# Optimization experiments

Measured on AMD Instinct MI355X. Metric: run time of the kernel, lower is better.

## Reference

```python
import jax, jax.numpy as jnp
import numpy as np

L_LAYERS, D, H, FF_MUL = 4, 512, 8, 4
VOCAB, SEQ, MEM, CMEM, RATIO = 32000, 1024, 1024, 256, 4
DH = D // H


def _ln(x, g, b):
    mu = jnp.mean(x, -1, keepdims=True)
    var = jnp.mean((x - mu) ** 2, -1, keepdims=True)
    return (x - mu) / jnp.sqrt(var + 1e-5) * g + b


def _heads(x):
    b, n, _ = x.shape
    return x.reshape(b, n, H, -1).transpose(0, 2, 1, 3)  # [b,h,n,dh]


def _shift(x):
    # relative-position shift trick, x: [b,h,i,j] -> [b,h,i,j]
    b, h, i, j = x.shape
    x = jnp.concatenate([x, jnp.zeros((b, h, i, i), x.dtype)], -1)
    l = i + j - 1
    x = x.reshape(b, h, i * (i + j))
    pad = (-x.shape[-1]) % l
    x = jnp.pad(x, ((0, 0), (0, 0), (0, pad))).reshape(b, h, -1, l)
    return x[:, :, :i, i - 1:]


def _conv(x, w, b):
    # x: [B,L,D], w: [D_out, D_in, RATIO] (OIH), stride=RATIO
    y = jax.lax.conv_general_dilated(x.transpose(0, 2, 1), w, (RATIO,), 'VALID',
                                     dimension_numbers=('NCH', 'OIH', 'NCH'))
    return y.transpose(0, 2, 1) + b


def _full_attn(q, k, v):
    dots = jnp.einsum('bhid,bhjd->bhij', q, k) * (q.shape[-1] ** -0.5)
    return jnp.einsum('bhij,bhjd->bhid', jax.nn.softmax(dots, -1), v)


def setup_inputs() -> dict:
    key = jax.random.key(0)
    ks = jax.random.split(key, 24)
    s = 0.02
    return {
        'seq': jax.random.randint(ks[0], (4, SEQ), 0, VOCAB),
        'mask': jnp.ones((4, SEQ), dtype=bool),
        'mems': jax.random.normal(ks[1], (L_LAYERS, 4, MEM, D)) * s,
        'cmems': jax.random.normal(ks[2], (L_LAYERS, 4, CMEM, D)) * s,
        'pos_emb': jax.random.normal(ks[3], (H, CMEM + MEM + SEQ, DH)) * s,
        'embed': jax.random.normal(ks[4], (VOCAB, D)) * s,
        'ln1_g': jnp.ones((L_LAYERS, D)), 'ln1_b': jnp.zeros((L_LAYERS, D)),
        'Wq': jax.random.normal(ks[5], (L_LAYERS, D, D)) * s,
        'Wkv': jax.random.normal(ks[6], (L_LAYERS, D, 2 * D)) * s,
        'Wo': jax.random.normal(ks[7], (L_LAYERS, D, D)) * s,
        'bo': jnp.zeros((L_LAYERS, D)),
        'conv_w': jax.random.normal(ks[8], (L_LAYERS, D, D, RATIO)) * s,
        'conv_b': jnp.zeros((L_LAYERS, D)),
        'ln2_g': jnp.ones((L_LAYERS, D)), 'ln2_b': jnp.zeros((L_LAYERS, D)),
        'W1': jax.random.normal(ks[9], (L_LAYERS, D, FF_MUL * D)) * s,
        'b1': jnp.zeros((L_LAYERS, FF_MUL * D)),
        'W2': jax.random.normal(ks[10], (L_LAYERS, FF_MUL * D, D)) * s,
        'b2': jnp.zeros((L_LAYERS, D)),
    }


def _forward(seq, mask, mems, cmems, pos_emb, embed, ln1_g, ln1_b, Wq, Wkv, Wo, bo,
             conv_w, conv_b, ln2_g, ln2_b, W1, b1, W2, b2):
    scale = DH ** -0.5
    x = embed[seq]  # [b,t,d]
    maskb = mask.astype(bool)
    new_mems, new_cmems = [], []
    aux_total = jnp.zeros((), x.dtype)
    w_acc = 0.0
    for l in range(L_LAYERS):
        mem, cmem = mems[l], cmems[l]
        xn = _ln(x, ln1_g[l], ln1_b[l])
        q = _heads(xn @ Wq[l])
        kv_in = jnp.concatenate([cmem, mem, xn], 1)  # [b,kv_len,d]
        kv_len = kv_in.shape[1]
        k, v = jnp.split(kv_in @ Wkv[l], 2, -1)
        k, v = _heads(k), _heads(v)
        dots = jnp.einsum('bhid,bhjd->bhij', q, k) * scale
        pe = pos_emb[:, -kv_len:]
        dots = dots + _shift(jnp.einsum('bhid,hjd->bhij', q, pe) * scale)
        m2 = maskb[:, None, :, None] & maskb[:, None, None, :]  # [b,1,t,t]
        m2 = jnp.pad(m2, ((0, 0), (0, 0), (0, 0), (kv_len - SEQ, 0)), constant_values=True)
        dots = jnp.where(m2, dots, -jnp.finfo(dots.dtype).max)
        attn = jax.nn.softmax(dots, -1)
        w_acc = w_acc + jnp.mean(jax.lax.stop_gradient(attn), axis=(0, 1))
        out = jnp.einsum('bhij,bhjd->bhid', attn, v)
        out = out.transpose(0, 2, 1, 3).reshape(x.shape[0], SEQ, D)
        x = x + out @ Wo[l] + bo[l]
        # FIFO memory update (queue normed x, evict oldest)
        queue = jnp.concatenate([mem, xn], 1)
        old_mem, new_mem = queue[:, :-MEM], queue[:, -MEM:]
        pad_amt = old_mem.shape[1] % RATIO
        if pad_amt:
            old_mem = jnp.pad(old_mem, ((0, 0), (pad_amt, 0), (0, 0)))
        comp = _conv(old_mem, conv_w[l], conv_b[l])
        new_cmem = jnp.concatenate([cmem, comp], 1)[:, -CMEM:]
        new_mems.append(new_mem)
        new_cmems.append(new_cmem)
        # reconstruction (attention-reconstruction) aux loss
        old_mem_d = jax.lax.stop_gradient(old_mem)
        comp2 = _conv(old_mem_d, conv_w[l], conv_b[l])
        ck, cv = jnp.split(comp2 @ jax.lax.stop_gradient(Wkv[l]), 2, -1)
        ck, cv = _heads(ck), _heads(cv)
        start = kv_len - min(mem.shape[1], MEM) - SEQ
        ok = jax.lax.stop_gradient(k[:, :, start:kv_len - SEQ])
        ov = jax.lax.stop_gradient(v[:, :, start:kv_len - SEQ])
        qd = jax.lax.stop_gradient(q)
        aux_total = aux_total + jnp.mean((_full_attn(qd, ok, ov) - _full_attn(qd, ck, cv)) ** 2)
        # feed-forward block (PreNorm + Residual), exact GELU like torch nn.GELU
        xn2 = _ln(x, ln2_g[l], ln2_b[l])
        x = x + jax.nn.gelu(xn2 @ W1[l] + b1[l], approximate=False) @ W2[l] + b2[l]
    return (x, jnp.stack(new_mems), jnp.stack(new_cmems),
            aux_total / L_LAYERS, w_acc / L_LAYERS)


def reference(seq, mask, mems, cmems, pos_emb, embed, ln1_g, ln1_b, Wq, Wkv, Wo, bo,
              conv_w, conv_b, ln2_g, ln2_b, W1, b1, W2, b2):
    return _forward(seq, mask, mems, cmems, pos_emb, embed, ln1_g, ln1_b, Wq, Wkv, Wo, bo,
                    conv_w, conv_b, ln2_g, ln2_b, W1, b1, W2, b2)
```

## Files before the change

### kernel.cpp

```cpp
#include <hip/hip_runtime.h>
#include <hip/hip_bf16.h>


typedef __hip_bfloat16 bf16;
typedef short s16x8 __attribute__((ext_vector_type(8)));
typedef float f32x4 __attribute__((ext_vector_type(4)));

__device__ __forceinline__ f32x4 mfma16(s16x8 a, s16x8 b, f32x4 c) {
  return __builtin_amdgcn_mfma_f32_16x16x32_bf16(a, b, c, 0, 0, 0);
}

typedef __attribute__((address_space(1))) const void gvoid;
typedef __attribute__((address_space(3))) void lvoid;
__device__ __forceinline__ void gll16(const void* g, void* l) {
  __builtin_amdgcn_global_load_lds((gvoid*)g, (lvoid*)l, 16, 0, 0);
}

__device__ __forceinline__ float b2f(unsigned short u) {
  return __uint_as_float(((unsigned)u) << 16);
}
__device__ __forceinline__ unsigned short f2bb(float f) {
  bf16 h = __float2bfloat16(f);
  return *reinterpret_cast<unsigned short*>(&h);
}
__device__ __forceinline__ float ldf(const float* p) { return *p; }
__device__ __forceinline__ float ldf(const bf16* p) { return __bfloat162float(*p); }
__device__ __forceinline__ float4 ld4(const float* p) { return *(const float4*)p; }
__device__ __forceinline__ float4 ld4(const bf16* p) {
  const ushort4 u = *(const ushort4*)p;
  return make_float4(b2f(u.x), b2f(u.y), b2f(u.z), b2f(u.w));
}
__device__ __forceinline__ void st4(float* p, float4 r) { *(float4*)p = r; }
__device__ __forceinline__ void st4(bf16* p, float4 r) {
  *(ushort4*)p = make_ushort4(f2bb(r.x), f2bb(r.y), f2bb(r.z), f2bb(r.w));
}
__device__ __forceinline__ void stf(float* p, float v) { *p = v; }
__device__ __forceinline__ void stf(bf16* p, float v) { *p = __float2bfloat16(v); }

__global__ void probe_k(const void* ln1g, unsigned* flag) {
  if (threadIdx.x == 0) {
    const unsigned short u = *(const unsigned short*)ln1g;
    *flag = (u == 0x3F80u) ? 1u : 0u;
  }
}

template <int BM, int AMODE, bool ADD, bool BIAS, bool GELU, typename TC>
__global__ __launch_bounds__(256) void mgemm_k(
    const bf16* __restrict__ A, const int lda, const bf16* __restrict__ Bt,
    TC* __restrict__ C, const int ldc, const float* __restrict__ bias,
    const int K) {
  constexpr int NF = (BM == 128) ? 4 : 2;
  __shared__ bf16 As[BM * 64];
  __shared__ bf16 Bs[128 * 64];
  const int t = threadIdx.x, w = t >> 6, lane = t & 63;
  const int g = lane >> 4, li = lane & 15;
  const int m0 = blockIdx.y * BM, n0 = blockIdx.x << 7;
  const int wrow = (BM == 128) ? ((w >> 1) << 6) : 0;
  const int wcol = (BM == 128) ? ((w & 1) << 6) : (w << 5);
  f32x4 acc[4][NF];
#pragma unroll
  for (int mf = 0; mf < 4; mf++)
#pragma unroll
    for (int nf = 0; nf < NF; nf++)
#pragma unroll
      for (int e = 0; e < 4; e++) acc[mf][nf][e] = 0.f;
  constexpr int ACH = BM / 32;
  const int srow = lane >> 3, s8 = lane & 7;
  for (int k0 = 0; k0 < K; k0 += 64) {
    __syncthreads();
#pragma unroll
    for (int it = 0; it < ACH; it++) {
      const int chunk = w * ACH + it;
      const int row = (chunk << 3) + srow;
      const int k8 = s8 ^ (row & 7);
      const bf16* src;
      if constexpr (AMODE == 0) {
        src = A + (size_t)(m0 + row) * lda + k0 + (k8 << 3);
      } else if constexpr (AMODE == 1) {
        const int m = m0 + row;
        src = A + ((size_t)((m >> 8) * 2304 + 256) << 9) + (m & 255) * 2048 +
              k0 + (k8 << 3);
      } else {
        const int m = m0 + row;
        src = A + ((size_t)((m >> 10) * 2304 + 1280 + (m & 1023)) << 9) + k0 +
              (k8 << 3);
      }
      gll16(src, As + (chunk << 9));
    }
#pragma unroll
    for (int it = 0; it < 4; it++) {
      const int chunk = (w << 2) + it;
      const int row = (chunk << 3) + srow;
      const int k8 = s8 ^ (row & 7);
      gll16(Bt + (size_t)(n0 + row) * K + k0 + (k8 << 3), Bs + (chunk << 9));
    }
    __syncthreads();
#pragma unroll
    for (int ks = 0; ks < 2; ks++) {
      s16x8 af[4];
#pragma unroll
      for (int mf = 0; mf < 4; mf++) {
        const int row = wrow + (mf << 4) + li;
        af[mf] = *reinterpret_cast<const s16x8*>(
            As + (row << 6) + ((((ks << 2) + g) ^ (row & 7)) << 3));
      }
#pragma unroll
      for (int nf = 0; nf < NF; nf++) {
        const int col = wcol + (nf << 4) + li;
        const s16x8 bfr = *reinterpret_cast<const s16x8*>(
            Bs + (col << 6) + ((((ks << 2) + g) ^ (col & 7)) << 3));
#pragma unroll
        for (int mf = 0; mf < 4; mf++)
          acc[mf][nf] = mfma16(af[mf], bfr, acc[mf][nf]);
      }
    }
  }
#pragma unroll
  for (int mf = 0; mf < 4; mf++)
#pragma unroll
    for (int nf = 0; nf < NF; nf++) {
      const int n = n0 + wcol + (nf << 4) + li;
      const float bv = BIAS ? bias[n] : 0.f;
#pragma unroll
      for (int r = 0; r < 4; r++) {
        const int m = m0 + wrow + (mf << 4) + (g << 2) + r;
        float v = acc[mf][nf][r] + bv;
        if constexpr (GELU) v = 0.5f * v * (1.0f + erff(v * 0.70710678118f));
        TC* cp = C + (size_t)m * ldc + n;
        if constexpr (ADD)
          *cp += v;
        else
          stf(cp, v);
      }
    }
}

__global__ __launch_bounds__(256) void flash_k(
    const bf16* __restrict__ q, const bf16* __restrict__ kbase,
    const bf16* __restrict__ vbase, const int kvlen, const int ldkv,
    const int bstride, const bf16* __restrict__ pe,
    const bf16* __restrict__ zrow, float2* __restrict__ ml,
    bf16* __restrict__ outp) {
  __shared__ short k_s[2][4096];
  __shared__ short v_s[2][4096];
  __shared__ short p_s[4096];
  const int t = threadIdx.x, w = t >> 6, lane = t & 63;
  const int g = lane >> 4, li = lane & 15;
  const int bid = blockIdx.x;
  const int h = bid & 7;
  const int sl = bid >> 3;
  const int b = sl >> 4;
  const int i0 = (sl & 15) << 6;
  const bf16* qp =
      q + (size_t)(b * 1024 + i0 + (w << 4) + li) * 512 + (h << 6) + (g << 3);
  const s16x8 qf0 = *reinterpret_cast<const s16x8*>(qp);
  const s16x8 qf1 = *reinterpret_cast<const s16x8*>(qp + 32);
  const bf16* kpb = kbase + (size_t)b * bstride + (h << 6);
  const bf16* vpb = vbase + (size_t)b * bstride + (h << 6);
  const bf16* peh = pe + (size_t)h * 147456;
  const int vr = t >> 3, vc8 = t & 7;
  const int kr = lane >> 3, kc8 = lane & 7;
  float mreg[4] = {-1e30f, -1e30f, -1e30f, -1e30f};
  float lreg[4] = {0.f, 0.f, 0.f, 0.f};
  f32x4 o[4];
#pragma unroll
  for (int nt = 0; nt < 4; nt++)
#pragma unroll
    for (int e = 0; e < 4; e++) o[nt][e] = 0.f;

#define STAGE_K(J0, BUF)                                                      \
  {                                                                           \
    _Pragma("unroll") for (int it = 0; it < 2; it++) {                        \
      const int chunk = (w << 1) + it;                                        \
      const int row = (chunk << 3) + kr;                                      \
      gll16(kpb + (size_t)((J0) + row) * ldkv + ((kc8 ^ (row & 7)) << 3),     \
            &k_s[BUF][chunk << 9]);                                           \
    }                                                                         \
  }
#define LOAD_V(J0, VA, VB)                                                    \
  {                                                                           \
    VA = *reinterpret_cast<const s16x8*>(                                     \
        vpb + (size_t)((J0) + vr) * ldkv + (vc8 << 3));                       \
    VB = *reinterpret_cast<const s16x8*>(                                     \
        vpb + (size_t)((J0) + 32 + vr) * ldkv + (vc8 << 3));                  \
  }
#define WRITE_V(BUF, VA, VB)                                                  \
  {                                                                           \
    _Pragma("unroll") for (int e = 0; e < 8; e++) {                           \
      const int d = (vc8 << 3) + e;                                           \
      const int sw = ((vc8 ^ e) & 7) << 3;                                    \
      v_s[BUF][((d << 6) + vr) ^ sw] = VA[e];                                 \
      v_s[BUF][((d << 6) + (vr + 32)) ^ sw] = VB[e];                          \
    }                                                                         \
  }

  {
    s16x8 va, vb2;
    STAGE_K(0, 0);
    LOAD_V(0, va, vb2);
    WRITE_V(0, va, vb2);
    __syncthreads();
  }
  int cur = 0;
  for (int j0 = 0; j0 < kvlen; j0 += 64) {
    const bool last = (j0 + 64 >= kvlen);
    s16x8 nva, nvb;
    if (!last) {
      LOAD_V(j0 + 64, nva, nvb);
      STAGE_K(j0 + 64, cur ^ 1);
    }
    const int ub0 = j0 - i0 + 960;
    const bool doT = (ub0 < 2304);
    s16x8 pb[5][2];
    if (doT) {
      const int ubase = j0 - i0 + 1008 - (w << 4);
#pragma unroll
      for (int ut = 0; ut < 5; ut++) {
        const int u = ubase + (ut << 4) + li;
        const bf16* pp = (u < 2304) ? peh + ((size_t)u << 6) : zrow;
        pb[ut][0] = *reinterpret_cast<const s16x8*>(pp + (g << 3));
        pb[ut][1] = *reinterpret_cast<const s16x8*>(pp + 32 + (g << 3));
      }
    }
    f32x4 s[4];
#pragma unroll
    for (int nt = 0; nt < 4; nt++) {
#pragma unroll
      for (int e = 0; e < 4; e++) s[nt][e] = 0.f;
      const int j = (nt << 4) + li;
      const s16x8 kb0 = *reinterpret_cast<const s16x8*>(
          &k_s[cur][(j << 6) + ((g ^ (j & 7)) << 3)]);
      const s16x8 kb1 = *reinterpret_cast<const s16x8*>(
          &k_s[cur][(j << 6) + (((g + 4) ^ (j & 7)) << 3)]);
      s[nt] = mfma16(qf0, kb0, s[nt]);
      s[nt] = mfma16(qf1, kb1, s[nt]);
    }
    if (doT) {
      f32x4 t5[5];
#pragma unroll
      for (int ut = 0; ut < 5; ut++) {
#pragma unroll
        for (int e = 0; e < 4; e++) t5[ut][e] = 0.f;
        t5[ut] = mfma16(qf0, pb[ut][0], t5[ut]);
        t5[ut] = mfma16(qf1, pb[ut][1], t5[ut]);
      }
#pragma unroll
      for (int r = 0; r < 4; r++) {
        const int il = (g << 2) + r;
        const int local = li - il + 15;
        const int srcl = (g << 4) | (local & 15);
        float tv[5];
#pragma unroll
        for (int ut = 0; ut < 5; ut++) tv[ut] = __shfl(t5[ut][r], srcl);
        const bool hi = local >= 16;
#pragma unroll
        for (int nt = 0; nt < 4; nt++) s[nt][r] += hi ? tv[nt + 1] : tv[nt];
      }
    }
#pragma unroll
    for (int nt = 0; nt < 4; nt++)
#pragma unroll
      for (int e = 0; e < 4; e++) s[nt][e] *= 0.125f;
    float pr[4][4];
#pragma unroll
    for (int r = 0; r < 4; r++) {
      float tm = fmaxf(fmaxf(s[0][r], s[1][r]), fmaxf(s[2][r], s[3][r]));
#pragma unroll
      for (int off = 1; off < 16; off <<= 1) tm = fmaxf(tm, __shfl_xor(tm, off));
      const float mn = fmaxf(mreg[r], tm);
      const float al = __expf(mreg[r] - mn);
      mreg[r] = mn;
      float te = 0.f;
#pragma unroll
      for (int nt = 0; nt < 4; nt++) {
        pr[nt][r] = __expf(s[nt][r] - mn);
        te += pr[nt][r];
      }
#pragma unroll
      for (int off = 1; off < 16; off <<= 1) te += __shfl_xor(te, off);
      lreg[r] = lreg[r] * al + te;
#pragma unroll
      for (int nt = 0; nt < 4; nt++) o[nt][r] *= al;
    }
    short* pw = p_s + (w << 10);
#pragma unroll
    for (int nt = 0; nt < 4; nt++)
#pragma unroll
      for (int r = 0; r < 4; r++) {
        const int il = (g << 2) + r;
        pw[((il << 6) + (nt << 4) + li) ^ ((il & 7) << 3)] = (short)f2bb(pr[nt][r]);
      }
#pragma unroll
    for (int ks = 0; ks < 2; ks++) {
      const s16x8 pa = *reinterpret_cast<const s16x8*>(
          pw + (((li << 6) + (ks << 5) + (g << 3)) ^ ((li & 7) << 3)));
#pragma unroll
      for (int nt = 0; nt < 4; nt++) {
        const int d = (nt << 4) + li;
        const s16x8 vb = *reinterpret_cast<const s16x8*>(
            &v_s[cur][((d << 6) + (ks << 5) + (g << 3)) ^
                      ((((d >> 3) ^ (d & 7)) & 7) << 3)]);
        o[nt] = mfma16(pa, vb, o[nt]);
      }
    }
    if (!last) WRITE_V(cur ^ 1, nva, nvb);
    __syncthreads();
    cur ^= 1;
  }
#undef STAGE_K
#undef LOAD_V
#undef WRITE_V
  float rl[4];
#pragma unroll
  for (int r = 0; r < 4; r++) rl[r] = 1.0f / lreg[r];
  if (li == 0) {
#pragma unroll
    for (int r = 0; r < 4; r++)
      ml[(size_t)((b << 3) + h) * 1024 + i0 + (w << 4) + (g << 2) + r] =
          make_float2(mreg[r], lreg[r]);
  }
#pragma unroll
  for (int nt = 0; nt < 4; nt++)
#pragma unroll
    for (int r = 0; r < 4; r++) {
      const size_t adr = (size_t)(b * 1024 + i0 + (w << 4) + (g << 2) + r) * 512 +
                         (h << 6) + (nt << 4) + li;
      stf(outp + adr, o[nt][r] * rl[r]);
    }
}

__global__ __launch_bounds__(256) void auxf_k(
    const bf16* __restrict__ q, const bf16* __restrict__ k1,
    const bf16* __restrict__ v1, const bf16* __restrict__ k2,
    const bf16* __restrict__ v2, float* __restrict__ auxsum) {
  __shared__ short k_s[4096];
  __shared__ short v_s[4096];
  __shared__ short p_s[4096];
  const int t = threadIdx.x, w = t >> 6, lane = t & 63;
  const int g = lane >> 4, li = lane & 15;
  const int bid = blockIdx.x;
  const int h = bid & 7;
  const int sl = bid >> 3;
  const int b = sl >> 4;
  const int i0 = (sl & 15) << 6;
  const bf16* qp =
      q + (size_t)(b * 1024 + i0 + (w << 4) + li) * 512 + (h << 6) + (g << 3);
  const s16x8 qf0 = *reinterpret_cast<const s16x8*>(qp);
  const s16x8 qf1 = *reinterpret_cast<const s16x8*>(qp + 32);
  const bf16* kbs[2] = {k1 + (size_t)b * 2359296 + (h << 6),
                        k2 + (size_t)b * 262144 + (h << 6)};
  const bf16* vbs[2] = {v1 + (size_t)b * 2359296 + (h << 6),
                        v2 + (size_t)b * 262144 + (h << 6)};
  const int vr = t >> 3, vc8 = t & 7;
  const int kr = lane >> 3, kc8 = lane & 7;
  float ms[2][4], ls[2][4];
  f32x4 o[2][4];
#pragma unroll
  for (int sg = 0; sg < 2; sg++)
#pragma unroll
    for (int r = 0; r < 4; r++) {
      ms[sg][r] = -1e30f;
      ls[sg][r] = 0.f;
#pragma unroll
      for (int e = 0; e < 4; e++) o[sg][r][e] = 0.f;
    }
#pragma unroll
  for (int sg = 0; sg < 2; sg++) {
    const bf16* kbp = kbs[sg];
    const bf16* vbp = vbs[sg];
    const int NT = sg ? 4 : 16;
    for (int jt = 0; jt < NT; jt++) {
      const int j0 = jt << 6;
      __syncthreads();
      {
#pragma unroll
        for (int it = 0; it < 2; it++) {
          const int chunk = (w << 1) + it;
          const int row = (chunk << 3) + kr;
          gll16(kbp + (size_t)(j0 + row) * 1024 + ((kc8 ^ (row & 7)) << 3),
                &k_s[chunk << 9]);
        }
        const s16x8 va = *reinterpret_cast<const s16x8*>(
            vbp + (size_t)(j0 + vr) * 1024 + (vc8 << 3));
        const s16x8 vb2 = *reinterpret_cast<const s16x8*>(
            vbp + (size_t)(j0 + 32 + vr) * 1024 + (vc8 << 3));
#pragma unroll
        for (int e = 0; e < 8; e++) {
          const int d = (vc8 << 3) + e;
          const int sw = ((vc8 ^ e) & 7) << 3;
          v_s[((d << 6) + vr) ^ sw] = va[e];
          v_s[((d << 6) + (vr + 32)) ^ sw] = vb2[e];
        }
      }
      __syncthreads();
      f32x4 s[4];
#pragma unroll
      for (int nt = 0; nt < 4; nt++) {
#pragma unroll
        for (int e = 0; e < 4; e++) s[nt][e] = 0.f;
        const int j = (nt << 4) + li;
        const s16x8 kb0 = *reinterpret_cast<const s16x8*>(
            &k_s[(j << 6) + ((g ^ (j & 7)) << 3)]);
        const s16x8 kb1 = *reinterpret_cast<const s16x8*>(
            &k_s[(j << 6) + (((g + 4) ^ (j & 7)) << 3)]);
        s[nt] = mfma16(qf0, kb0, s[nt]);
        s[nt] = mfma16(qf1, kb1, s[nt]);
      }
      float pr[4][4];
#pragma unroll
      for (int r = 0; r < 4; r++) {
        float sv[4];
#pragma unroll
        for (int nt = 0; nt < 4; nt++) sv[nt] = s[nt][r] * 0.125f;
        float tm = fmaxf(fmaxf(sv[0], sv[1]), fmaxf(sv[2], sv[3]));
#pragma unroll
        for (int off = 1; off < 16; off <<= 1) tm = fmaxf(tm, __shfl_xor(tm, off));
        const float mn = fmaxf(ms[sg][r], tm);
        const float al = __expf(ms[sg][r] - mn);
        ms[sg][r] = mn;
        float te = 0.f;
#pragma unroll
        for (int nt = 0; nt < 4; nt++) {
          pr[nt][r] = __expf(sv[nt] - mn);
          te += pr[nt][r];
        }
#pragma unroll
        for (int off = 1; off < 16; off <<= 1) te += __shfl_xor(te, off);
        ls[sg][r] = ls[sg][r] * al + te;
#pragma unroll
        for (int nt = 0; nt < 4; nt++) o[sg][nt][r] *= al;
      }
      short* pw = p_s + (w << 10);
#pragma unroll
      for (int nt = 0; nt < 4; nt++)
#pragma unroll
        for (int r = 0; r < 4; r++) {
          const int il = (g << 2) + r;
          pw[((il << 6) + (nt << 4) + li) ^ ((il & 7) << 3)] =
              (short)f2bb(pr[nt][r]);
        }
#pragma unroll
      for (int ks = 0; ks < 2; ks++) {
        const s16x8 pa = *reinterpret_cast<const s16x8*>(
            pw + (((li << 6) + (ks << 5) + (g << 3)) ^ ((li & 7) << 3)));
#pragma unroll
        for (int nt = 0; nt < 4; nt++) {
          const int d = (nt << 4) + li;
          const s16x8 vb = *reinterpret_cast<const s16x8*>(
              &v_s[((d << 6) + (ks << 5) + (g << 3)) ^
                   ((((d >> 3) ^ (d & 7)) & 7) << 3)]);
          o[sg][nt] = mfma16(pa, vb, o[sg][nt]);
        }
      }
    }
  }
  float rl0[4], rl1[4];
#pragma unroll
  for (int r = 0; r < 4; r++) {
    rl0[r] = 1.0f / ls[0][r];
    rl1[r] = 1.0f / ls[1][r];
  }
  float sq = 0.f;
#pragma unroll
  for (int nt = 0; nt < 4; nt++)
#pragma unroll
    for (int r = 0; r < 4; r++) {
      const float dv = o[0][nt][r] * rl0[r] - o[1][nt][r] * rl1[r];
      sq = fmaf(dv, dv, sq);
    }
#pragma unroll
  for (int off = 1; off < 64; off <<= 1) sq += __shfl_xor(sq, off);
  float* fl = reinterpret_cast<float*>(p_s);
  __syncthreads();
  if (lane == 0) fl[w] = sq;
  __syncthreads();
  if (t == 0) atomicAdd(auxsum, fl[0] + fl[1] + fl[2] + fl[3]);
}

__global__ __launch_bounds__(256) void wacc_k(const bf16* __restrict__ q,
                                              const bf16* __restrict__ kv,
                                              const bf16* __restrict__ pe,
                                              const bf16* __restrict__ zrow,
                                              const float2* __restrict__ ml,
                                              float* __restrict__ w_acc) {
  __shared__ short k_s[2][4096];
  const int t = threadIdx.x, w = t >> 6, lane = t & 63;
  const int g = lane >> 4, li = lane & 15;
  const int bid = blockIdx.x;
  const int xcd = bid & 7, idx = bid >> 3;
  const int j0t = ((idx >> 4) << 3) + xcd;
  if (j0t >= 36) return;
  const int i0 = (idx & 15) << 6, j0 = j0t << 6;
  const int ub0 = j0 - i0 + 960;
  const bool doT = (ub0 < 2304);
  const int kr = lane >> 3, kc8 = lane & 7;
  f32x4 acc[4];
#pragma unroll
  for (int nt = 0; nt < 4; nt++)
#pragma unroll
    for (int e = 0; e < 4; e++) acc[nt][e] = 0.f;

#define STAGE_KW(HB, BUF)                                                     \
  {                                                                           \
    const int hh = (HB) >> 2, bb = (HB)&3;                                    \
    const bf16* kpb = kv + (size_t)bb * 2359296 + (hh << 6);                  \
    _Pragma("unroll") for (int it = 0; it < 2; it++) {                        \
      const int chunk = (w << 1) + it;                                        \
      const int row = (chunk << 3) + kr;                                      \
      gll16(kpb + (size_t)(j0 + row) * 1024 + ((kc8 ^ (row & 7)) << 3),       \
            &k_s[BUF][chunk << 9]);                                           \
    }                                                                         \
  }
#define LOADQ(HB, Q0, Q1)                                                     \
  {                                                                           \
    const int hh = (HB) >> 2, bb = (HB)&3;                                    \
    const bf16* qpp = q + (size_t)(bb * 1024 + i0 + (w << 4) + li) * 512 +    \
                      (hh << 6) + (g << 3);                                   \
    Q0 = *reinterpret_cast<const s16x8*>(qpp);                                \
    Q1 = *reinterpret_cast<const s16x8*>(qpp + 32);                           \
  }
#define LOADML(HB, DST)                                                       \
  {                                                                           \
    const int hh = (HB) >> 2, bb = (HB)&3;                                    \
    _Pragma("unroll") for (int r = 0; r < 4; r++) DST[r] =                    \
        ml[(size_t)((bb << 3) + hh) * 1024 + i0 + (w << 4) + (g << 2) + r];   \
  }

  STAGE_KW(0, 0);
  s16x8 qf0, qf1;
  float2 mlr[4];
  LOADQ(0, qf0, qf1);
  LOADML(0, mlr);
  s16x8 pb[5][2];
  __syncthreads();
  int cur = 0;
  for (int hb = 0; hb < 32; hb++) {
    const int h = hb >> 2;
    if (hb < 31) STAGE_KW(hb + 1, cur ^ 1);
    if (doT && (hb & 3) == 0) {
      const bf16* peh = pe + (size_t)h * 147456;
      const int ubase = j0 - i0 + 1008 - (w << 4);
#pragma unroll
      for (int ut = 0; ut < 5; ut++) {
        const int u = ubase + (ut << 4) + li;
        const bf16* pp = (u < 2304) ? peh + ((size_t)u << 6) : zrow;
        pb[ut][0] = *reinterpret_cast<const s16x8*>(pp + (g << 3));
        pb[ut][1] = *reinterpret_cast<const s16x8*>(pp + 32 + (g << 3));
      }
    }
    s16x8 qn0, qn1;
    float2 mln[4];
    if (hb < 31) {
      LOADQ(hb + 1, qn0, qn1);
      LOADML(hb + 1, mln);
    }
    f32x4 s[4];
#pragma unroll
    for (int nt = 0; nt < 4; nt++) {
#pragma unroll
      for (int e = 0; e < 4; e++) s[nt][e] = 0.f;
      const int j = (nt << 4) + li;
      const s16x8 kb0 = *reinterpret_cast<const s16x8*>(
          &k_s[cur][(j << 6) + ((g ^ (j & 7)) << 3)]);
      const s16x8 kb1 = *reinterpret_cast<const s16x8*>(
          &k_s[cur][(j << 6) + (((g + 4) ^ (j & 7)) << 3)]);
      s[nt] = mfma16(qf0, kb0, s[nt]);
      s[nt] = mfma16(qf1, kb1, s[nt]);
    }
    if (doT) {
      f32x4 t5[5];
#pragma unroll
      for (int ut = 0; ut < 5; ut++) {
#pragma unroll
        for (int e = 0; e < 4; e++) t5[ut][e] = 0.f;
        t5[ut] = mfma16(qf0, pb[ut][0], t5[ut]);
        t5[ut] = mfma16(qf1, pb[ut][1], t5[ut]);
      }
#pragma unroll
      for (int r = 0; r < 4; r++) {
        const int il = (g << 2) + r;
        const int local = li - il + 15;
        const int srcl = (g << 4) | (local & 15);
        float tv[5];
#pragma unroll
        for (int ut = 0; ut < 5; ut++) tv[ut] = __shfl(t5[ut][r], srcl);
        const bool hi = local >= 16;
#pragma unroll
        for (int nt = 0; nt < 4; nt++) s[nt][r] += hi ? tv[nt + 1] : tv[nt];
      }
    }
#pragma unroll
    for (int r = 0; r < 4; r++) {
      const float rr = 1.0f / mlr[r].y;
#pragma unroll
      for (int nt = 0; nt < 4; nt++)
        acc[nt][r] += __expf(s[nt][r] * 0.125f - mlr[r].x) * rr;
    }
    __syncthreads();
    cur ^= 1;
    if (hb < 31) {
      qf0 = qn0;
      qf1 = qn1;
#pragma unroll
      for (int r = 0; r < 4; r++) mlr[r] = mln[r];
    }
  }
#undef STAGE_KW
#undef LOADQ
#undef LOADML
#pragma unroll
  for (int nt = 0; nt < 4; nt++)
#pragma unroll
    for (int r = 0; r < 4; r++) {
      float* wp = w_acc + (size_t)(i0 + (w << 4) + (g << 2) + r) * 2304 + j0 +
                  (nt << 4) + li;
      *wp += acc[nt][r];
    }
}

template <typename TIN>
__global__ __launch_bounds__(256) void wtr_k(
    const TIN* __restrict__ Wq, const TIN* __restrict__ Wkv,
    const TIN* __restrict__ Wo, const TIN* __restrict__ W1,
    const TIN* __restrict__ W2, bf16* __restrict__ WT,
    const unsigned* flag, unsigned want) {
  if (*flag != want) return;
  __shared__ bf16 tile[64][65];
  int bx = blockIdx.x;
  const TIN* W;
  bf16* dst;
  int N, K;
  if (bx < 64) {
    W = Wq; dst = WT; N = 512; K = 512;
  } else if (bx < 192) {
    W = Wkv; dst = WT + 262144; N = 1024; K = 512; bx -= 64;
  } else if (bx < 256) {
    W = Wo; dst = WT + 786432; N = 512; K = 512; bx -= 192;
  } else if (bx < 512) {
    W = W1; dst = WT + 1048576; N = 2048; K = 512; bx -= 256;
  } else {
    W = W2; dst = WT + 2097152; N = 512; K = 2048; bx -= 512;
  }
  const int tn = N >> 6;
  const int kt = bx / tn, nt = bx - kt * tn;
  const int k0 = kt << 6, n0 = nt << 6;
  const int t = threadIdx.x;
#pragma unroll
  for (int i = 0; i < 16; i++) {
    const int idx = (i << 8) + t;
    const int kr = idx >> 6, nc = idx & 63;
    tile[kr][nc] = __float2bfloat16(ldf(W + (size_t)(k0 + kr) * N + n0 + nc));
  }
  __syncthreads();
#pragma unroll
  for (int i = 0; i < 16; i++) {
    const int idx = (i << 8) + t;
    const int nr = idx >> 6, kc = idx & 63;
    dst[(size_t)(n0 + nr) * K + k0 + kc] = tile[kc][nr];
  }
}

template <typename TIN>
__global__ void wcp_k(const TIN* __restrict__ cw, bf16* __restrict__ WcT,
                      const unsigned* flag, unsigned want) {
  if (*flag != want) return;
  const int id = blockIdx.x * 256 + threadIdx.x;
  const int o = id >> 11, p = id & 2047;
  const int r = p >> 9, i = p & 511;
  WcT[id] = __float2bfloat16(ldf(cw + ((size_t)o << 11) + (i << 2) + r));
}

template <typename TIN>
__global__ void kvb_k(const TIN* __restrict__ cmem, const TIN* __restrict__ mem,
                      bf16* __restrict__ kvin, const unsigned* flag, unsigned want) {
  if (*flag != want) return;
  const int id = blockIdx.x * 256 + threadIdx.x;
  const int row = id >> 7, c4 = (id & 127) << 2;
  const int b = row / 1280, j = row - b * 1280;
  const TIN* src = (j < 256) ? cmem + (((size_t)(b * 256 + j)) << 9) + c4
                             : mem + (((size_t)(b * 1024 + j - 256)) << 9) + c4;
  st4(kvin + (((size_t)(b * 2304 + j)) << 9) + c4, ld4(src));
}

template <typename TIN>
__global__ void bcvt_k(const TIN* __restrict__ bo, const TIN* __restrict__ cb,
                       const TIN* __restrict__ b1, const TIN* __restrict__ b2,
                       float* __restrict__ bws, const unsigned* flag, unsigned want) {
  if (*flag != want) return;
  const int id = blockIdx.x * 256 + threadIdx.x;
  const int l = id / 3584, r = id - l * 3584;
  float v;
  if (r < 512) v = ldf(bo + l * 512 + r);
  else if (r < 1024) v = ldf(cb + l * 512 + r - 512);
  else if (r < 3072) v = ldf(b1 + l * 2048 + r - 1024);
  else v = ldf(b2 + l * 512 + r - 3072);
  bws[id] = v;
}

template <typename TIN, typename TY>
__global__ __launch_bounds__(256) void ln_k(const float* __restrict__ x,
                                            const TIN* __restrict__ g,
                                            const TIN* __restrict__ bta,
                                            TY* __restrict__ y, bf16* kvx,
                                            const unsigned* flag, unsigned want) {
  if (*flag != want) return;
  const int w = threadIdx.x >> 6, lane = threadIdx.x & 63;
  const size_t row = (size_t)blockIdx.x * 4 + w;
  const float* xr = x + row * 512;
  float v[8], s = 0, ss = 0;
#pragma unroll
  for (int i = 0; i < 8; i++) {
    v[i] = xr[lane + (i << 6)];
    s += v[i];
    ss = fmaf(v[i], v[i], ss);
  }
#pragma unroll
  for (int off = 1; off < 64; off <<= 1) {
    s += __shfl_xor(s, off);
    ss += __shfl_xor(ss, off);
  }
  const float mu = s * (1.0f / 512.0f);
  const float var = ss * (1.0f / 512.0f) - mu * mu;
  const float inv = rsqrtf(var + 1e-5f);
  bf16* k2 = kvx ? kvx + (((row >> 10) * 2304 + 1280 + (row & 1023)) << 9) : nullptr;
#pragma unroll
  for (int i = 0; i < 8; i++) {
    const int c = lane + (i << 6);
    const float val = (v[i] - mu) * inv * ldf(g + c) + ldf(bta + c);
    stf(y + row * 512 + c, val);
    if (k2) k2[c] = __float2bfloat16(val);
  }
}

template <typename TIN>
__global__ void embed_k(const int* __restrict__ seq, const TIN* __restrict__ emb,
                        float* __restrict__ x, const unsigned* flag, unsigned want) {
  if (*flag != want) return;
  const int row = blockIdx.x;
  const int tok = seq[row];
  const TIN* e = emb + (size_t)tok * 512;
  float* xr = x + (size_t)row * 512;
  for (int c = threadIdx.x; c < 512; c += 256) xr[c] = ldf(e + c);
}

template <typename TIN>
__global__ void cvtpe_k(const TIN* __restrict__ pe, bf16* __restrict__ peb,
                        const unsigned* flag, unsigned want) {
  if (*flag != want) return;
  const int i = blockIdx.x * 256 + threadIdx.x;
  peb[i] = __float2bfloat16(ldf(pe + i));
}

__global__ void zero_k(float* __restrict__ p, int n) {
  for (int i = blockIdx.x * 256 + threadIdx.x; i < n; i += gridDim.x * 256) p[i] = 0.0f;
}

template <typename TOUT>
__global__ void cpy_k(const bf16* __restrict__ s, TOUT* __restrict__ d, int n,
                      const unsigned* flag, unsigned want) {
  if (*flag != want) return;
  for (int i = blockIdx.x * 256 + threadIdx.x; i < n; i += gridDim.x * 256)
    stf(d + i, ldf(s + i));
}

template <typename TOUT>
__global__ void f2bs_k(const float* __restrict__ s, TOUT* __restrict__ d, float sc,
                       int n, const unsigned* flag, unsigned want) {
  if (*flag != want) return;
  for (int i = blockIdx.x * 256 + threadIdx.x; i < n; i += gridDim.x * 256)
    stf(d + i, s[i] * sc);
}

template <typename TOUT>
__global__ void fin_aux_k(const float* __restrict__ acc, TOUT* __restrict__ d,
                          const unsigned* flag, unsigned want) {
  if (*flag != want) return;
  if (threadIdx.x == 0) stf(d, acc[0] * (1.0f / 8388608.0f));
}

extern "C" void kernel_launch(void* const* d_in, const int* in_sizes, int n_in,
                              void* d_out, int out_size, void* d_ws, size_t ws_size,
                              hipStream_t stream) {
  typedef const bf16 CB;
  typedef const float CF;
  const int* seq = (const int*)d_in[0];
  CB *mems_b = (CB*)d_in[2], *cmems_b = (CB*)d_in[3], *pe_b = (CB*)d_in[4],
     *emb_b = (CB*)d_in[5], *l1g_b = (CB*)d_in[6], *l1b_b = (CB*)d_in[7],
     *Wq_b = (CB*)d_in[8], *Wkv_b = (CB*)d_in[9], *Wo_b = (CB*)d_in[10],
     *bo_b = (CB*)d_in[11], *cw_b = (CB*)d_in[12], *cb_b = (CB*)d_in[13],
     *l2g_b = (CB*)d_in[14], *l2b_b = (CB*)d_in[15], *W1_b = (CB*)d_in[16],
     *b1_b = (CB*)d_in[17], *W2_b = (CB*)d_in[18], *b2_b = (CB*)d_in[19];
  CF *mems_f = (CF*)d_in[2], *cmems_f = (CF*)d_in[3], *pe_f = (CF*)d_in[4],
     *emb_f = (CF*)d_in[5], *l1g_f = (CF*)d_in[6], *l1b_f = (CF*)d_in[7],
     *Wq_f = (CF*)d_in[8], *Wkv_f = (CF*)d_in[9], *Wo_f = (CF*)d_in[10],
     *bo_f = (CF*)d_in[11], *cw_f = (CF*)d_in[12], *cb_f = (CF*)d_in[13],
     *l2g_f = (CF*)d_in[14], *l2b_f = (CF*)d_in[15], *W1_f = (CF*)d_in[16],
     *b1_f = (CF*)d_in[17], *W2_f = (CF*)d_in[18], *b2_f = (CF*)d_in[19];
  bf16* outb = (bf16*)d_out;
  float* outf = (float*)d_out;

  float* ws = (float*)d_ws;
  float* x = ws;
  bf16* q = (bf16*)(ws + 2097152);
  bf16* kv = (bf16*)(ws + 3145728);
  bf16* mid = (bf16*)(ws + 3145728);
  float* region = ws + 7864320;
  bf16* attn_o = (bf16*)region;
  bf16* xn2 = (bf16*)region;
  bf16* ckcv = (bf16*)(ws + 9961472);
  float* w_acc = ws + 10485760;
  bf16* cmp_ws = (bf16*)(ws + 12845056);
  float2* ml = (float2*)(ws + 13369344);
  float* auxsum = ws + 13434880;
  unsigned* flag = (unsigned*)(ws + 13434881);
  bf16* pe_w = (bf16*)(ws + 13434884);
  float* bias_ws = ws + 14024708;
  bf16* kvin = (bf16*)(ws + 14039044);
  bf16* WT = (bf16*)(ws + 16398340);
  float* zrow_f = ws + 18757636;
  bf16* zrow = (bf16*)zrow_f;

  probe_k<<<1, 64, 0, stream>>>(d_in[6], flag);
  zero_k<<<2048, 256, 0, stream>>>(w_acc, 2359296);
  zero_k<<<1, 256, 0, stream>>>(auxsum, 1);
  zero_k<<<1, 64, 0, stream>>>(zrow_f, 32);
  embed_k<bf16><<<4096, 256, 0, stream>>>(seq, emb_b, x, flag, 1);
  embed_k<float><<<4096, 256, 0, stream>>>(seq, emb_f, x, flag, 0);
  cvtpe_k<bf16><<<4608, 256, 0, stream>>>(pe_b, pe_w, flag, 1);
  cvtpe_k<float><<<4608, 256, 0, stream>>>(pe_f, pe_w, flag, 0);
  bcvt_k<bf16><<<56, 256, 0, stream>>>(bo_b, cb_b, b1_b, b2_b, bias_ws, flag, 1);
  bcvt_k<float><<<56, 256, 0, stream>>>(bo_f, cb_f, b1_f, b2_f, bias_ws, flag, 0);

  for (int l = 0; l < 4; l++) {
    bf16* xnl_b = outb + 2097152 + (size_t)l * 2097152;
    float* xnl_f = outf + 2097152 + (size_t)l * 2097152;
    bf16* cmp_b = outb + 10485760 + (size_t)l * 524288;
    float* cmp_f = outf + 10485760 + (size_t)l * 524288;
    const float* bl = bias_ws + l * 3584;

    wtr_k<bf16><<<768, 256, 0, stream>>>(Wq_b + (size_t)l * 262144,
        Wkv_b + (size_t)l * 524288, Wo_b + (size_t)l * 262144,
        W1_b + (size_t)l * 1048576, W2_b + (size_t)l * 1048576, WT, flag, 1);
    wtr_k<float><<<768, 256, 0, stream>>>(Wq_f + (size_t)l * 262144,
        Wkv_f + (size_t)l * 524288, Wo_f + (size_t)l * 262144,
        W1_f + (size_t)l * 1048576, W2_f + (size_t)l * 1048576, WT, flag, 0);
    wcp_k<bf16><<<4096, 256, 0, stream>>>(cw_b + (size_t)l * 1048576, WT + 3145728, flag, 1);
    wcp_k<float><<<4096, 256, 0, stream>>>(cw_f + (size_t)l * 1048576, WT + 3145728, flag, 0);
    kvb_k<bf16><<<2560, 256, 0, stream>>>(cmems_b + (size_t)l * 524288,
                                          mems_b + (size_t)l * 2097152, kvin, flag, 1);
    kvb_k<float><<<2560, 256, 0, stream>>>(cmems_f + (size_t)l * 524288,
                                           mems_f + (size_t)l * 2097152, kvin, flag, 0);
    ln_k<bf16, bf16><<<1024, 256, 0, stream>>>(x, l1g_b + l * 512, l1b_b + l * 512,
                                               xnl_b, kvin, flag, 1);
    ln_k<float, float><<<1024, 256, 0, stream>>>(x, l1g_f + l * 512, l1b_f + l * 512,
                                                 xnl_f, kvin, flag, 0);
    mgemm_k<64, 2, false, false, false, bf16><<<dim3(4, 64), 256, 0, stream>>>(
        kvin, 512, WT, q, 512, nullptr, 512);
    mgemm_k<128, 0, false, false, false, bf16><<<dim3(8, 72), 256, 0, stream>>>(
        kvin, 512, WT + 262144, kv, 1024, nullptr, 512);
    flash_k<<<512, 256, 0, stream>>>(q, kv, kv + 512, 2304, 1024, 2359296,
                                     pe_w, zrow, ml, attn_o);
    wacc_k<<<640, 256, 0, stream>>>(q, kv, pe_w, zrow, ml, w_acc);
    mgemm_k<64, 0, true, true, false, float><<<dim3(4, 64), 256, 0, stream>>>(
        attn_o, 512, WT + 786432, x, 512, bl, 512);
    mgemm_k<64, 1, false, true, false, bf16><<<dim3(4, 16), 256, 0, stream>>>(
        kvin, 0, WT + 3145728, cmp_ws, 512, bl + 512, 2048);
    cpy_k<bf16><<<512, 256, 0, stream>>>(cmp_ws, cmp_b, 524288, flag, 1);
    cpy_k<float><<<512, 256, 0, stream>>>(cmp_ws, cmp_f, 524288, flag, 0);
    mgemm_k<64, 0, false, false, false, bf16><<<dim3(8, 16), 256, 0, stream>>>(
        cmp_ws, 512, WT + 262144, ckcv, 1024, nullptr, 512);
    auxf_k<<<512, 256, 0, stream>>>(q, kv + 262144, kv + 262144 + 512,
                                    ckcv, ckcv + 512, auxsum);
    ln_k<bf16, bf16><<<1024, 256, 0, stream>>>(x, l2g_b + l * 512, l2b_b + l * 512,
                                               xn2, nullptr, flag, 1);
    ln_k<float, bf16><<<1024, 256, 0, stream>>>(x, l2g_f + l * 512, l2b_f + l * 512,
                                                xn2, nullptr, flag, 0);
    mgemm_k<128, 0, false, true, true, bf16><<<dim3(16, 32), 256, 0, stream>>>(
        xn2, 512, WT + 1048576, mid, 2048, bl + 1024, 512);
    mgemm_k<64, 0, true, true, false, float><<<dim3(4, 64), 256, 0, stream>>>(
        mid, 2048, WT + 2097152, x, 512, bl + 3072, 2048);
  }

  f2bs_k<bf16><<<2048, 256, 0, stream>>>(x, outb, 1.0f, 2097152, flag, 1);
  f2bs_k<float><<<2048, 256, 0, stream>>>(x, outf, 1.0f, 2097152, flag, 0);
  f2bs_k<bf16><<<2048, 256, 0, stream>>>(w_acc, outb + 12582913, 1.0f / 128.0f, 2359296, flag, 1);
  f2bs_k<float><<<2048, 256, 0, stream>>>(w_acc, outf + 12582913, 1.0f / 128.0f, 2359296, flag, 0);
  fin_aux_k<bf16><<<1, 64, 0, stream>>>(auxsum, outb + 12582912, flag, 1);
  fin_aux_k<float><<<1, 64, 0, stream>>>(auxsum, outf + 12582912, flag, 0);
}
```

Baseline: 2.049 ms.

## Split flash attention over KV halves with merge kernel; split wacc over heads

The flash attention kernel now splits the 2304-long KV range into two halves, launching twice as many blocks. Each block writes unnormalized fp32 partial outputs and (max, sum) stats, and a new merge kernel combines them with log-sum-exp rescaling into bf16 output and final stats. The wacc kernel is likewise split across two halves of the head/batch loop and accumulates with atomicAdd. The aim is to raise occupancy on a 512-block launch, at the cost of extra fp32 partial traffic, an additional kernel launch and atomic contention.

Result: slower. 2.162 ms (+5.6%).

```diff
diff --git a/kernel.cpp b/kernel.cpp
--- a/kernel.cpp
+++ b/kernel.cpp
@@ -137,10 +137,9 @@
 
 __global__ __launch_bounds__(256) void flash_k(
     const bf16* __restrict__ q, const bf16* __restrict__ kbase,
-    const bf16* __restrict__ vbase, const int kvlen, const int ldkv,
-    const int bstride, const bf16* __restrict__ pe,
-    const bf16* __restrict__ zrow, float2* __restrict__ ml,
-    bf16* __restrict__ outp) {
+    const bf16* __restrict__ vbase, const bf16* __restrict__ pe,
+    const bf16* __restrict__ zrow, float2* __restrict__ ml_part,
+    float* __restrict__ o_part) {
   __shared__ short k_s[2][4096];
   __shared__ short v_s[2][4096];
   __shared__ short p_s[4096];
@@ -149,14 +148,16 @@
   const int bid = blockIdx.x;
   const int h = bid & 7;
   const int sl = bid >> 3;
-  const int b = sl >> 4;
-  const int i0 = (sl & 15) << 6;
+  const int sp = sl & 1;
+  const int i0 = ((sl >> 1) & 15) << 6;
+  const int b = sl >> 5;
+  const int jlo = sp * 1152, jhi = jlo + 1152;
   const bf16* qp =
       q + (size_t)(b * 1024 + i0 + (w << 4) + li) * 512 + (h << 6) + (g << 3);
   const s16x8 qf0 = *reinterpret_cast<const s16x8*>(qp);
   const s16x8 qf1 = *reinterpret_cast<const s16x8*>(qp + 32);
-  const bf16* kpb = kbase + (size_t)b * bstride + (h << 6);
-  const bf16* vpb = vbase + (size_t)b * bstride + (h << 6);
+  const bf16* kpb = kbase + (size_t)b * 2359296 + (h << 6);
+  const bf16* vpb = vbase + (size_t)b * 2359296 + (h << 6);
   const bf16* peh = pe + (size_t)h * 147456;
   const int vr = t >> 3, vc8 = t & 7;
   const int kr = lane >> 3, kc8 = lane & 7;
@@ -173,16 +174,16 @@
     _Pragma("unroll") for (int it = 0; it < 2; it++) {                        \
       const int chunk = (w << 1) + it;                                        \
       const int row = (chunk << 3) + kr;                                      \
-      gll16(kpb + (size_t)((J0) + row) * ldkv + ((kc8 ^ (row & 7)) << 3),     \
+      gll16(kpb + (size_t)((J0) + row) * 1024 + ((kc8 ^ (row & 7)) << 3),     \
             &k_s[BUF][chunk << 9]);                                           \
     }                                                                         \
   }
 #define LOAD_V(J0, VA, VB)                                                    \
   {                                                                           \
     VA = *reinterpret_cast<const s16x8*>(                                     \
-        vpb + (size_t)((J0) + vr) * ldkv + (vc8 << 3));                       \
+        vpb + (size_t)((J0) + vr) * 1024 + (vc8 << 3));                       \
     VB = *reinterpret_cast<const s16x8*>(                                     \
-        vpb + (size_t)((J0) + 32 + vr) * ldkv + (vc8 << 3));                  \
+        vpb + (size_t)((J0) + 32 + vr) * 1024 + (vc8 << 3));                  \
   }
 #define WRITE_V(BUF, VA, VB)                                                  \
   {                                                                           \
@@ -196,14 +197,14 @@
 
   {
     s16x8 va, vb2;
-    STAGE_K(0, 0);
-    LOAD_V(0, va, vb2);
+    STAGE_K(jlo, 0);
+    LOAD_V(jlo, va, vb2);
     WRITE_V(0, va, vb2);
     __syncthreads();
   }
   int cur = 0;
-  for (int j0 = 0; j0 < kvlen; j0 += 64) {
-    const bool last = (j0 + 64 >= kvlen);
+  for (int j0 = jlo; j0 < jhi; j0 += 64) {
+    const bool last = (j0 + 64 >= jhi);
     s16x8 nva, nvb;
     if (!last) {
       LOAD_V(j0 + 64, nva, nvb);
@@ -310,23 +311,46 @@
 #undef STAGE_K
 #undef LOAD_V
 #undef WRITE_V
-  float rl[4];
-#pragma unroll
-  for (int r = 0; r < 4; r++) rl[r] = 1.0f / lreg[r];
   if (li == 0) {
 #pragma unroll
     for (int r = 0; r < 4; r++)
-      ml[(size_t)((b << 3) + h) * 1024 + i0 + (w << 4) + (g << 2) + r] =
-          make_float2(mreg[r], lreg[r]);
+      ml_part[(size_t)((sp << 5) + (b << 3) + h) * 1024 + i0 + (w << 4) +
+              (g << 2) + r] = make_float2(mreg[r], lreg[r]);
   }
 #pragma unroll
   for (int nt = 0; nt < 4; nt++)
 #pragma unroll
     for (int r = 0; r < 4; r++) {
-      const size_t adr = (size_t)(b * 1024 + i0 + (w << 4) + (g << 2) + r) * 512 +
-                         (h << 6) + (nt << 4) + li;
-      stf(outp + adr, o[nt][r] * rl[r]);
-    }
+      const size_t adr =
+          (size_t)((sp * 4 + b) * 1024 + i0 + (w << 4) + (g << 2) + r) * 512 +
+          (h << 6) + (nt << 4) + li;
+      o_part[adr] = o[nt][r];
+    }
+}
+
+__global__ __launch_bounds__(256) void merge_k(const float* __restrict__ o_part,
+                                               const float2* __restrict__ mlp,
+                                               bf16* __restrict__ out,
+                                               float2* __restrict__ mlf) {
+  const int id = blockIdx.x * 256 + threadIdx.x;
+  const int row = id >> 7, c4 = (id & 127) << 2;
+  const int b = row >> 10, i = row & 1023, h = c4 >> 6;
+  const size_t mlrow = (size_t)((b << 3) + h) * 1024 + i;
+  const float2 s1 = mlp[mlrow];
+  const float2 s2 = mlp[32768 + mlrow];
+  const float m = fmaxf(s1.x, s2.x);
+  const float w1 = __expf(s1.x - m), w2 = __expf(s2.x - m);
+  const float l = w1 * s1.y + w2 * s2.y;
+  const float rl = 1.0f / l;
+  const float4 a = *(const float4*)(o_part + (size_t)row * 512 + c4);
+  const float4 bq = *(const float4*)(o_part + 2097152 + (size_t)row * 512 + c4);
+  float4 r;
+  r.x = (w1 * a.x + w2 * bq.x) * rl;
+  r.y = (w1 * a.y + w2 * bq.y) * rl;
+  r.z = (w1 * a.z + w2 * bq.z) * rl;
+  r.w = (w1 * a.w + w2 * bq.w) * rl;
+  st4(out + (size_t)row * 512 + c4, r);
+  if ((c4 & 63) == 0) mlf[mlrow] = make_float2(m, l);
 }
 
 __global__ __launch_bounds__(256) void auxf_k(
@@ -487,10 +511,14 @@
   const int t = threadIdx.x, w = t >> 6, lane = t & 63;
   const int g = lane >> 4, li = lane & 15;
   const int bid = blockIdx.x;
-  const int xcd = bid & 7, idx = bid >> 3;
+  const int xcd = bid & 7;
+  int idx = bid >> 3;
+  const int hs = idx & 1;
+  idx >>= 1;
   const int j0t = ((idx >> 4) << 3) + xcd;
   if (j0t >= 36) return;
   const int i0 = (idx & 15) << 6, j0 = j0t << 6;
+  const int hb0 = hs << 4, hend = hb0 + 16;
   const int ub0 = j0 - i0 + 960;
   const bool doT = (ub0 < 2304);
   const int kr = lane >> 3, kc8 = lane & 7;
@@ -526,17 +554,18 @@
         ml[(size_t)((bb << 3) + hh) * 1024 + i0 + (w << 4) + (g << 2) + r];   \
   }
 
-  STAGE_KW(0, 0);
+  STAGE_KW(hb0, 0);
   s16x8 qf0, qf1;
   float2 mlr[4];
-  LOADQ(0, qf0, qf1);
-  LOADML(0, mlr);
+  LOADQ(hb0, qf0, qf1);
+  LOADML(hb0, mlr);
   s16x8 pb[5][2];
   __syncthreads();
   int cur = 0;
-  for (int hb = 0; hb < 32; hb++) {
+  for (int hb = hb0; hb < hend; hb++) {
     const int h = hb >> 2;
-    if (hb < 31) STAGE_KW(hb + 1, cur ^ 1);
+    const bool more = (hb + 1 < hend);
+    if (more) STAGE_KW(hb + 1, cur ^ 1);
     if (doT && (hb & 3) == 0) {
       const bf16* peh = pe + (size_t)h * 147456;
       const int ubase = j0 - i0 + 1008 - (w << 4);
@@ -550,7 +579,7 @@
     }
     s16x8 qn0, qn1;
     float2 mln[4];
-    if (hb < 31) {
+    if (more) {
       LOADQ(hb + 1, qn0, qn1);
       LOADML(hb + 1, mln);
     }
@@ -598,7 +627,7 @@
     }
     __syncthreads();
     cur ^= 1;
-    if (hb < 31) {
+    if (more) {
       qf0 = qn0;
       qf1 = qn1;
 #pragma unroll
@@ -614,7 +643,7 @@
     for (int r = 0; r < 4; r++) {
       float* wp = w_acc + (size_t)(i0 + (w << 4) + (g << 2) + r) * 2304 + j0 +
                   (nt << 4) + li;
-      *wp += acc[nt][r];
+      atomicAdd(wp, acc[nt][r]);
     }
 }
 
@@ -819,6 +848,8 @@
   bf16* WT = (bf16*)(ws + 16398340);
   float* zrow_f = ws + 18757636;
   bf16* zrow = (bf16*)zrow_f;
+  float* o_part = ws + 18757668;
+  float2* ml_part = (float2*)(ws + 22951972);
 
   probe_k<<<1, 64, 0, stream>>>(d_in[6], flag);
   zero_k<<<2048, 256, 0, stream>>>(w_acc, 2359296);
@@ -858,9 +889,10 @@
         kvin, 512, WT, q, 512, nullptr, 512);
     mgemm_k<128, 0, false, false, false, bf16><<<dim3(8, 72), 256, 0, stream>>>(
         kvin, 512, WT + 262144, kv, 1024, nullptr, 512);
-    flash_k<<<512, 256, 0, stream>>>(q, kv, kv + 512, 2304, 1024, 2359296,
-                                     pe_w, zrow, ml, attn_o);
-    wacc_k<<<640, 256, 0, stream>>>(q, kv, pe_w, zrow, ml, w_acc);
+    flash_k<<<1024, 256, 0, stream>>>(q, kv, kv + 512, pe_w, zrow,
+                                      ml_part, o_part);
+    merge_k<<<2048, 256, 0, stream>>>(o_part, ml_part, attn_o, ml);
+    wacc_k<<<1280, 256, 0, stream>>>(q, kv, pe_w, zrow, ml, w_acc);
     mgemm_k<64, 0, true, true, false, float><<<dim3(4, 64), 256, 0, stream>>>(
         attn_o, 512, WT + 786432, x, 512, bl, 512);
     mgemm_k<64, 1, false, true, false, bf16><<<dim3(4, 16), 256, 0, stream>>>(
```
